# Optimization experiments

Hardware: AMD Instinct MI355X
Metric: run time of the kernel (lower is better)

The kernel has to match this reference:

```python
import jax, jax.numpy as jnp
import numpy as np

NUM_HEADS = 16
MASKED_BIAS = -10000.0


def setup_inputs() -> dict:
    key = jax.random.key(0)
    k1, k2, k3 = jax.random.split(key, 3)
    B, S, D = 4, 2048, 1024
    scale = 0.02
    return {
        "hidden_states": jax.random.normal(k1, (B, S, D), dtype=jnp.float32),
        "c_attn_w": jax.random.normal(k2, (D, 3 * D), dtype=jnp.float32) * scale,
        "c_attn_b": jnp.zeros((3 * D,), dtype=jnp.float32),
        "c_proj_w": jax.random.normal(k3, (D, D), dtype=jnp.float32) * scale,
        "c_proj_b": jnp.zeros((D,), dtype=jnp.float32),
    }


def reference(hidden_states, c_attn_w, c_attn_b, c_proj_w, c_proj_b):
    B, S, D = hidden_states.shape
    H = NUM_HEADS
    hd = D // H
    # qkv projection (HF Conv1D: x @ W + b)
    qkv = hidden_states @ c_attn_w + c_attn_b  # [B, S, 3D]
    q, k, v = jnp.split(qkv, 3, axis=-1)

    def split_heads(t):
        return t.reshape(B, S, H, hd).transpose(0, 2, 1, 3)  # [B, H, S, hd]

    q, k, v = split_heads(q), split_heads(k), split_heads(v)
    # full score matrix [B, H, S, S] (eager attention)
    attn = jnp.einsum("bhqd,bhkd->bhqk", q, k) / jnp.sqrt(jnp.float32(hd))
    causal = jnp.tril(jnp.ones((S, S), dtype=bool))  # [S, S]
    attn = jnp.where(causal[None, None], attn, jnp.float32(MASKED_BIAS))
    attn = jax.nn.softmax(attn, axis=-1)
    out = jnp.einsum("bhqk,bhkd->bhqd", attn, v)  # [B, H, S, hd]
    out = out.transpose(0, 2, 1, 3).reshape(B, S, D)  # merge heads
    out = out @ c_proj_w + c_proj_b
    return out
```

## Files before the change

kernel.cpp:

```cpp
#include <hip/hip_runtime.h>

#define NH 16
#define HD 64

typedef __attribute__((ext_vector_type(8))) _Float16 f16x8;
typedef __attribute__((ext_vector_type(4))) float f32x4;
typedef __attribute__((ext_vector_type(8))) unsigned short us8;
typedef __attribute__((ext_vector_type(4))) unsigned short us4;
typedef __attribute__((ext_vector_type(2))) unsigned int u32x2;

#define CEXP 0.18033688f

__device__ __forceinline__ unsigned short f2h(float f) {
    _Float16 h = (_Float16)f;
    return __builtin_bit_cast(unsigned short, h);
}

__global__ __launch_bounds__(256)
void cast_f16(const float* __restrict__ in, unsigned short* __restrict__ out) {
    size_t i = ((size_t)blockIdx.x * 256 + threadIdx.x) * 4;
    float4 v = *reinterpret_cast<const float4*>(in + i);
    us4 w;
    w[0] = f2h(v.x); w[1] = f2h(v.y); w[2] = f2h(v.z); w[3] = f2h(v.w);
    *reinterpret_cast<us4*>(out + i) = w;
}

__global__ __launch_bounds__(256)
void transpose_cast(const float* __restrict__ in, unsigned short* __restrict__ out,
                    int R, int C) {
    __shared__ float T[64][65];
    const int c0 = blockIdx.x * 64, r0 = blockIdx.y * 64;
    const int tid = threadIdx.x;
    const int rr = tid >> 4, cc4 = (tid & 15) * 4;
    #pragma unroll
    for (int p = 0; p < 4; ++p) {
        int r = rr + p * 16;
        float4 v = *reinterpret_cast<const float4*>(
            in + (size_t)(r0 + r) * C + c0 + cc4);
        T[r][cc4] = v.x; T[r][cc4 + 1] = v.y; T[r][cc4 + 2] = v.z; T[r][cc4 + 3] = v.w;
    }
    __syncthreads();
    #pragma unroll
    for (int p = 0; p < 4; ++p) {
        int orow = rr + p * 16;
        us4 w;
        #pragma unroll
        for (int j = 0; j < 4; ++j) w[j] = f2h(T[cc4 + j][orow]);
        *reinterpret_cast<us4*>(out + (size_t)(c0 + orow) * R + r0 + cc4) = w;
    }
}

__device__ __forceinline__ void stage128(unsigned short* dst,
                                         const unsigned short* src, int stride) {
    const int tid = threadIdx.x;
    #pragma unroll
    for (int p = 0; p < 4; ++p) {
        int idx = tid + p * 256;
        int r = idx >> 3;
        int slot = idx & 7;
        us8 v = *reinterpret_cast<const us8*>(src + (size_t)r * stride + slot * 8);
        int cb = (slot << 4) ^ ((r & 7) << 4);
        *reinterpret_cast<us8*>(reinterpret_cast<char*>(dst) + r * 128 + cb) = v;
    }
}

__device__ __forceinline__ void stage64(unsigned short* dst,
                                        const unsigned short* src, int stride) {
    const int tid = threadIdx.x;
    #pragma unroll
    for (int p = 0; p < 2; ++p) {
        int idx = tid + p * 256;
        int r = idx >> 3;
        int slot = idx & 7;
        us8 v = *reinterpret_cast<const us8*>(src + (size_t)r * stride + slot * 8);
        int cb = (slot << 4) ^ ((r & 7) << 4);
        *reinterpret_cast<us8*>(reinterpret_cast<char*>(dst) + r * 128 + cb) = v;
    }
}

__device__ __forceinline__ f16x8 frag16(const unsigned short* base, int row0, int ks) {
    const int lane = threadIdx.x & 63;
    const int r = row0 + (lane & 15);
    int cb = ((ks << 6) + (lane & 48)) ^ ((r & 7) << 4);
    return *reinterpret_cast<const f16x8*>(
        reinterpret_cast<const char*>(base) + r * 128 + cb);
}

template<int MODE>
__global__ __launch_bounds__(256)
void gemm_f16(const unsigned short* __restrict__ A,
              const unsigned short* __restrict__ Bt,
              const float* __restrict__ bias,
              float* __restrict__ C,
              unsigned short* __restrict__ qb,
              unsigned short* __restrict__ kb,
              unsigned short* __restrict__ vtb,
              int M, int N, int K) {
    __shared__ __align__(16) unsigned short As[128 * 64];
    __shared__ __align__(16) unsigned short Bs[128 * 64];

    const int tid = threadIdx.x;
    const int wid = tid >> 6, lane = tid & 63, g = lane >> 4;
    const int wr = wid >> 1, wc = wid & 1;
    const int m0 = blockIdx.y * 128, n0 = blockIdx.x * 128;

    f32x4 acc[4][4];
    #pragma unroll
    for (int i = 0; i < 4; ++i)
        #pragma unroll
        for (int j = 0; j < 4; ++j) {
            acc[i][j][0] = 0.f; acc[i][j][1] = 0.f;
            acc[i][j][2] = 0.f; acc[i][j][3] = 0.f;
        }

    for (int k0 = 0; k0 < K; k0 += 64) {
        __syncthreads();
        stage128(As, A + (size_t)m0 * K + k0, K);
        stage128(Bs, Bt + (size_t)n0 * K + k0, K);
        __syncthreads();

        f16x8 af[4][2], bf[4][2];
        #pragma unroll
        for (int mi = 0; mi < 4; ++mi)
            #pragma unroll
            for (int ks = 0; ks < 2; ++ks)
                af[mi][ks] = frag16(As, wr * 64 + mi * 16, ks);
        #pragma unroll
        for (int ni = 0; ni < 4; ++ni)
            #pragma unroll
            for (int ks = 0; ks < 2; ++ks)
                bf[ni][ks] = frag16(Bs, wc * 64 + ni * 16, ks);

        __builtin_amdgcn_s_setprio(1);
        #pragma unroll
        for (int ks = 0; ks < 2; ++ks)
            #pragma unroll
            for (int mi = 0; mi < 4; ++mi)
                #pragma unroll
                for (int ni = 0; ni < 4; ++ni)
                    acc[mi][ni] = __builtin_amdgcn_mfma_f32_16x16x32_f16(
                        af[mi][ks], bf[ni][ks], acc[mi][ni], 0, 0, 0);
        __builtin_amdgcn_s_setprio(0);
    }

    const int colBase = n0 + wc * 64;
    const int rowBase = m0 + wr * 64;

    if (MODE == 0) {
        #pragma unroll
        for (int ni = 0; ni < 4; ++ni) {
            int col = colBase + ni * 16 + (lane & 15);
            float bv = bias[col];
            #pragma unroll
            for (int mi = 0; mi < 4; ++mi) {
                int row = rowBase + mi * 16 + g * 4;
                #pragma unroll
                for (int reg = 0; reg < 4; ++reg)
                    C[(size_t)(row + reg) * N + col] = acc[mi][ni][reg] + bv;
            }
        }
    } else {
        #pragma unroll
        for (int ni = 0; ni < 4; ++ni) {
            int col = colBase + ni * 16 + (lane & 15);
            float bv = bias[col];
            int seg = col >> 10;
            int cc = col & 1023;
            int h = cc >> 6, d = cc & 63;
            const float sc = (seg == 0) ? CEXP : 1.0f;
            #pragma unroll
            for (int mi = 0; mi < 4; ++mi) {
                int row = rowBase + mi * 16 + g * 4;
                int b = row >> 11, s = row & 2047;
                size_t bh = (size_t)(b * NH + h);
                if (seg < 2) {
                    unsigned short* dst = (seg ? kb : qb)
                        + bh * 2048 * 64 + (size_t)s * 64 + d;
                    #pragma unroll
                    for (int reg = 0; reg < 4; ++reg)
                        dst[(size_t)reg * 64] = f2h((acc[mi][ni][reg] + bv) * sc);
                } else {
                    unsigned short* dst = vtb
                        + bh * 64 * 2048 + (size_t)d * 2048 + s;
                    us4 w;
                    #pragma unroll
                    for (int reg = 0; reg < 4; ++reg)
                        w[reg] = f2h(acc[mi][ni][reg] + bv);
                    *reinterpret_cast<us4*>(dst) = w;
                }
            }
        }
    }
}

template<bool DIAG>
__device__ __forceinline__ void attn_tile(
    f16x8 qf0, f16x8 qf1,
    const unsigned short* Ks, const unsigned short* Vs, unsigned short* Pw,
    f32x4 (&o)[4], float& l_,
    int kt, int qrow_base, int lane, int g) {

    f32x4 s[4];
    #pragma unroll
    for (int n = 0; n < 4; ++n) { s[n][0] = 0.f; s[n][1] = 0.f; s[n][2] = 0.f; s[n][3] = 0.f; }

    __builtin_amdgcn_s_setprio(1);
    #pragma unroll
    for (int ks = 0; ks < 2; ++ks) {
        f16x8 b = ks ? qf1 : qf0;
        #pragma unroll
        for (int n = 0; n < 4; ++n)
            s[n] = __builtin_amdgcn_mfma_f32_16x16x32_f16(
                frag16(Ks, n * 16, ks), b, s[n], 0, 0, 0);
    }
    __builtin_amdgcn_s_setprio(0);

    const int q = lane & 15;
    float psum = 0.f;
    #pragma unroll
    for (int n = 0; n < 4; ++n) {
        float p0 = __builtin_exp2f(s[n][0]);
        float p1 = __builtin_exp2f(s[n][1]);
        float p2 = __builtin_exp2f(s[n][2]);
        float p3 = __builtin_exp2f(s[n][3]);
        if (DIAG) {
            const int kb_ = kt * 64 + (g << 2) + 16 * n;
            const int qg = qrow_base + q;
            p0 = (kb_ + 0 > qg) ? 0.f : p0;
            p1 = (kb_ + 1 > qg) ? 0.f : p1;
            p2 = (kb_ + 2 > qg) ? 0.f : p2;
            p3 = (kb_ + 3 > qg) ? 0.f : p3;
        }
        psum += (p0 + p1) + (p2 + p3);
        u32x2 w;
        w[0] = __builtin_bit_cast(unsigned int, __builtin_amdgcn_cvt_pkrtz(p0, p1));
        w[1] = __builtin_bit_cast(unsigned int, __builtin_amdgcn_cvt_pkrtz(p2, p3));
        int pcb = ((n << 5) + (g << 3)) ^ ((q & 7) << 4);
        *reinterpret_cast<u32x2*>(
            reinterpret_cast<char*>(Pw) + q * 128 + pcb) = w;
    }
    l_ += psum;

    __builtin_amdgcn_s_setprio(1);
    #pragma unroll
    for (int ks = 0; ks < 2; ++ks) {
        f16x8 pa = frag16(Pw, 0, ks);
        #pragma unroll
        for (int n = 0; n < 4; ++n)
            o[n] = __builtin_amdgcn_mfma_f32_16x16x32_f16(
                pa, frag16(Vs, n * 16, ks), o[n], 0, 0, 0);
    }
    __builtin_amdgcn_s_setprio(0);
}

__global__ __launch_bounds__(256, 4)
void attn_mfma(const unsigned short* __restrict__ qb,
               const unsigned short* __restrict__ kb,
               const unsigned short* __restrict__ vtb,
               unsigned short* __restrict__ attno) {
    const int f = blockIdx.x;
    const int xcd = f & 7;
    const int wi = f >> 3;
    const int bh = xcd * 8 + (wi >> 4);
    const int pair = wi & 15;
    const int qtA = pair, qtB = 31 - pair;
    const int tid = threadIdx.x;
    const int wid = tid >> 6, lane = tid & 63, g = lane >> 4;

    __shared__ __align__(16) unsigned short Ks[64 * 64];
    __shared__ __align__(16) unsigned short Vs[64 * 64];
    __shared__ __align__(16) unsigned short Ps[4][16 * 64];

    const unsigned short* kg0 = kb + (size_t)bh * 2048 * 64;
    const unsigned short* vg0 = vtb + (size_t)bh * 64 * 2048;

    const int qrl = wid * 16 + (lane & 15);
    const int qd0 = (lane >> 4) * 8;
    const unsigned short* qbase = qb + (size_t)bh * 2048 * 64;
    f16x8 qA0 = *reinterpret_cast<const f16x8*>(qbase + (size_t)(qtA * 64 + qrl) * 64 + qd0);
    f16x8 qA1 = *reinterpret_cast<const f16x8*>(qbase + (size_t)(qtA * 64 + qrl) * 64 + 32 + qd0);
    f16x8 qB0 = *reinterpret_cast<const f16x8*>(qbase + (size_t)(qtB * 64 + qrl) * 64 + qd0);
    f16x8 qB1 = *reinterpret_cast<const f16x8*>(qbase + (size_t)(qtB * 64 + qrl) * 64 + 32 + qd0);

    f32x4 oA[4], oB[4];
    float lA = 0.f, lB = 0.f;
    #pragma unroll
    for (int n = 0; n < 4; ++n) {
        #pragma unroll
        for (int r = 0; r < 4; ++r) { oA[n][r] = 0.f; oB[n][r] = 0.f; }
    }

    unsigned short* Pw = Ps[wid];
    const int qrbA = qtA * 64 + wid * 16;
    const int qrbB = qtB * 64 + wid * 16;

    auto STAGE = [&](int kt) {
        __syncthreads();
        stage64(Ks, kg0 + (size_t)kt * 64 * 64, 64);
        stage64(Vs, vg0 + (size_t)kt * 64, 2048);
        __syncthreads();
    };

    for (int kt = 0; kt < qtA; ++kt) {
        STAGE(kt);
        attn_tile<false>(qB0, qB1, Ks, Vs, Pw, oB, lB, kt, qrbB, lane, g);
        attn_tile<false>(qA0, qA1, Ks, Vs, Pw, oA, lA, kt, qrbA, lane, g);
    }
    STAGE(qtA);
    attn_tile<false>(qB0, qB1, Ks, Vs, Pw, oB, lB, qtA, qrbB, lane, g);
    attn_tile<true >(qA0, qA1, Ks, Vs, Pw, oA, lA, qtA, qrbA, lane, g);
    for (int kt = qtA + 1; kt < qtB; ++kt) {
        STAGE(kt);
        attn_tile<false>(qB0, qB1, Ks, Vs, Pw, oB, lB, kt, qrbB, lane, g);
    }
    STAGE(qtB);
    attn_tile<true >(qB0, qB1, Ks, Vs, Pw, oB, lB, qtB, qrbB, lane, g);

    const int b = bh >> 4, h = bh & 15;
    #pragma unroll
    for (int ph = 0; ph < 2; ++ph) {
        const int qt = ph ? qtB : qtA;
        f32x4* o = ph ? oB : oA;
        float ltot = ph ? lB : lA;
        ltot += __shfl_xor(ltot, 16);
        ltot += __shfl_xor(ltot, 32);
        unsigned short* ob = attno
            + (size_t)(b * 2048 + qt * 64 + wid * 16) * 1024 + h * 64;
        #pragma unroll
        for (int reg = 0; reg < 4; ++reg) {
            int row = (g << 2) + reg;
            float inv = 1.0f / __shfl(ltot, row);
            #pragma unroll
            for (int n = 0; n < 4; ++n)
                ob[(size_t)row * 1024 + n * 16 + (lane & 15)] = f2h(o[n][reg] * inv);
        }
    }
}

extern "C" void kernel_launch(void* const* d_in, const int* in_sizes, int n_in,
                              void* d_out, int out_size, void* d_ws, size_t ws_size,
                              hipStream_t stream) {
    const float* x    = (const float*)d_in[0];
    const float* Wqkv = (const float*)d_in[1];
    const float* bqkv = (const float*)d_in[2];
    const float* Wp   = (const float*)d_in[3];
    const float* bp   = (const float*)d_in[4];
    float* out = (float*)d_out;

    const int B = 4, S = 2048, D = 1024;
    const int M = B * S;
    const size_t HSZ = (size_t)M * D;

    unsigned short* xh    = (unsigned short*)d_ws;
    unsigned short* wqt   = xh + HSZ;
    unsigned short* wpt   = wqt + (size_t)3 * D * D;
    unsigned short* qbuf  = wpt + (size_t)D * D;
    unsigned short* kbuf  = qbuf + HSZ;
    unsigned short* vtb   = kbuf + HSZ;
    unsigned short* attno = vtb + HSZ;

    dim3 blk(256);
    cast_f16<<<dim3((int)(HSZ / 1024)), blk, 0, stream>>>(x, xh);
    transpose_cast<<<dim3(3 * D / 64, D / 64), blk, 0, stream>>>(Wqkv, wqt, D, 3 * D);
    transpose_cast<<<dim3(D / 64, D / 64), blk, 0, stream>>>(Wp, wpt, D, D);

    gemm_f16<1><<<dim3(3 * D / 128, M / 128), blk, 0, stream>>>(
        xh, wqt, bqkv, nullptr, qbuf, kbuf, vtb, M, 3 * D, D);
    attn_mfma<<<dim3(1024), blk, 0, stream>>>(qbuf, kbuf, vtb, attno);
    gemm_f16<0><<<dim3(D / 128, M / 128), blk, 0, stream>>>(
        attno, wpt, bp, out, nullptr, nullptr, nullptr, M, D, D);
}
```

Before: 182.9 us.

## Fuse input cast into QKV GEMM and double-buffer attention K/V via async LDS loads

Removes the standalone fp32->fp16 cast kernel by converting x on the fly while staging A tiles in the QKV GEMM. The attention kernel now double-buffers K and V tiles using global_load_lds direct-to-LDS loads with source-side swizzling, prefetching the next tile while computing the current one and cutting barriers per tile. Trade-offs: the GEMM reads fp32 activations (twice the bytes per A tile, repeated across column blocks), and uses round-toward-zero conversion.

Result: slower. 228.3 us (+24.8%).

```diff
diff --git a/kernel.cpp b/kernel.cpp
--- a/kernel.cpp
+++ b/kernel.cpp
@@ -16,14 +16,9 @@
     return __builtin_bit_cast(unsigned short, h);
 }
 
-__global__ __launch_bounds__(256)
-void cast_f16(const float* __restrict__ in, unsigned short* __restrict__ out) {
-    size_t i = ((size_t)blockIdx.x * 256 + threadIdx.x) * 4;
-    float4 v = *reinterpret_cast<const float4*>(in + i);
-    us4 w;
-    w[0] = f2h(v.x); w[1] = f2h(v.y); w[2] = f2h(v.z); w[3] = f2h(v.w);
-    *reinterpret_cast<us4*>(out + i) = w;
-}
+#define GL16(gp, lp) __builtin_amdgcn_global_load_lds(                        \
+    (const __attribute__((address_space(1))) void*)(gp),                      \
+    (__attribute__((address_space(3))) void*)(lp), 16, 0, 0)
 
 __global__ __launch_bounds__(256)
 void transpose_cast(const float* __restrict__ in, unsigned short* __restrict__ out,
@@ -64,17 +59,24 @@
     }
 }
 
-__device__ __forceinline__ void stage64(unsigned short* dst,
-                                        const unsigned short* src, int stride) {
-    const int tid = threadIdx.x;
-    #pragma unroll
-    for (int p = 0; p < 2; ++p) {
+__device__ __forceinline__ void stage128_f32(unsigned short* dst,
+                                             const float* src, int stride) {
+    const int tid = threadIdx.x;
+    #pragma unroll
+    for (int p = 0; p < 4; ++p) {
         int idx = tid + p * 256;
         int r = idx >> 3;
         int slot = idx & 7;
-        us8 v = *reinterpret_cast<const us8*>(src + (size_t)r * stride + slot * 8);
+        const float* s = src + (size_t)r * stride + slot * 8;
+        float4 a = *reinterpret_cast<const float4*>(s);
+        float4 b = *reinterpret_cast<const float4*>(s + 4);
+        uint4 w;
+        w.x = __builtin_bit_cast(unsigned int, __builtin_amdgcn_cvt_pkrtz(a.x, a.y));
+        w.y = __builtin_bit_cast(unsigned int, __builtin_amdgcn_cvt_pkrtz(a.z, a.w));
+        w.z = __builtin_bit_cast(unsigned int, __builtin_amdgcn_cvt_pkrtz(b.x, b.y));
+        w.w = __builtin_bit_cast(unsigned int, __builtin_amdgcn_cvt_pkrtz(b.z, b.w));
         int cb = (slot << 4) ^ ((r & 7) << 4);
-        *reinterpret_cast<us8*>(reinterpret_cast<char*>(dst) + r * 128 + cb) = v;
+        *reinterpret_cast<uint4*>(reinterpret_cast<char*>(dst) + r * 128 + cb) = w;
     }
 }
 
@@ -88,7 +90,7 @@
 
 template<int MODE>
 __global__ __launch_bounds__(256)
-void gemm_f16(const unsigned short* __restrict__ A,
+void gemm_f16(const void* __restrict__ Ax,
               const unsigned short* __restrict__ Bt,
               const float* __restrict__ bias,
               float* __restrict__ C,
@@ -115,7 +117,10 @@
 
     for (int k0 = 0; k0 < K; k0 += 64) {
         __syncthreads();
-        stage128(As, A + (size_t)m0 * K + k0, K);
+        if (MODE == 1)
+            stage128_f32(As, (const float*)Ax + (size_t)m0 * K + k0, K);
+        else
+            stage128(As, (const unsigned short*)Ax + (size_t)m0 * K + k0, K);
         stage128(Bs, Bt + (size_t)n0 * K + k0, K);
         __syncthreads();
 
@@ -267,12 +272,12 @@
     const int tid = threadIdx.x;
     const int wid = tid >> 6, lane = tid & 63, g = lane >> 4;
 
-    __shared__ __align__(16) unsigned short Ks[64 * 64];
-    __shared__ __align__(16) unsigned short Vs[64 * 64];
+    __shared__ __align__(16) unsigned short Ks[2][64 * 64];
+    __shared__ __align__(16) unsigned short Vs[2][64 * 64];
     __shared__ __align__(16) unsigned short Ps[4][16 * 64];
 
-    const unsigned short* kg0 = kb + (size_t)bh * 2048 * 64;
-    const unsigned short* vg0 = vtb + (size_t)bh * 64 * 2048;
+    const char* kg0 = (const char*)(kb + (size_t)bh * 2048 * 64);
+    const char* vg0 = (const char*)(vtb + (size_t)bh * 64 * 2048);
 
     const int qrl = wid * 16 + (lane & 15);
     const int qd0 = (lane >> 4) * 8;
@@ -294,27 +299,42 @@
     const int qrbA = qtA * 64 + wid * 16;
     const int qrbB = qtB * 64 + wid * 16;
 
-    auto STAGE = [&](int kt) {
+    auto PREF = [&](int kt, int buf) {
+        const char* kb_ = kg0 + (size_t)kt * 8192;
+        const char* vb_ = vg0 + (size_t)kt * 128;
+        #pragma unroll
+        for (int i = 0; i < 2; ++i) {
+            int rbase = wid * 16 + i * 8;
+            int row = rbase + (lane >> 3);
+            int gs = (lane & 7) ^ (row & 7);
+            GL16(kb_ + (size_t)row * 128 + gs * 16,
+                 (char*)Ks[buf] + rbase * 128);
+            GL16(vb_ + (size_t)row * 4096 + gs * 16,
+                 (char*)Vs[buf] + rbase * 128);
+        }
+    };
+
+    PREF(0, 0);
+    __syncthreads();
+    int cur = 0;
+    for (int kt = 0; kt <= qtB; ++kt) {
+        if (kt < qtB) PREF(kt + 1, cur ^ 1);
+        const unsigned short* Kc = Ks[cur];
+        const unsigned short* Vc = Vs[cur];
+        if (kt < qtA) {
+            attn_tile<false>(qB0, qB1, Kc, Vc, Pw, oB, lB, kt, qrbB, lane, g);
+            attn_tile<false>(qA0, qA1, Kc, Vc, Pw, oA, lA, kt, qrbA, lane, g);
+        } else if (kt == qtA) {
+            attn_tile<false>(qB0, qB1, Kc, Vc, Pw, oB, lB, kt, qrbB, lane, g);
+            attn_tile<true >(qA0, qA1, Kc, Vc, Pw, oA, lA, kt, qrbA, lane, g);
+        } else if (kt < qtB) {
+            attn_tile<false>(qB0, qB1, Kc, Vc, Pw, oB, lB, kt, qrbB, lane, g);
+        } else {
+            attn_tile<true >(qB0, qB1, Kc, Vc, Pw, oB, lB, kt, qrbB, lane, g);
+        }
         __syncthreads();
-        stage64(Ks, kg0 + (size_t)kt * 64 * 64, 64);
-        stage64(Vs, vg0 + (size_t)kt * 64, 2048);
-        __syncthreads();
-    };
-
-    for (int kt = 0; kt < qtA; ++kt) {
-        STAGE(kt);
-        attn_tile<false>(qB0, qB1, Ks, Vs, Pw, oB, lB, kt, qrbB, lane, g);
-        attn_tile<false>(qA0, qA1, Ks, Vs, Pw, oA, lA, kt, qrbA, lane, g);
-    }
-    STAGE(qtA);
-    attn_tile<false>(qB0, qB1, Ks, Vs, Pw, oB, lB, qtA, qrbB, lane, g);
-    attn_tile<true >(qA0, qA1, Ks, Vs, Pw, oA, lA, qtA, qrbA, lane, g);
-    for (int kt = qtA + 1; kt < qtB; ++kt) {
-        STAGE(kt);
-        attn_tile<false>(qB0, qB1, Ks, Vs, Pw, oB, lB, kt, qrbB, lane, g);
-    }
-    STAGE(qtB);
-    attn_tile<true >(qB0, qB1, Ks, Vs, Pw, oB, lB, qtB, qrbB, lane, g);
+        cur ^= 1;
+    }
 
     const int b = bh >> 4, h = bh & 15;
     #pragma unroll
@@ -351,8 +371,7 @@
     const int M = B * S;
     const size_t HSZ = (size_t)M * D;
 
-    unsigned short* xh    = (unsigned short*)d_ws;
-    unsigned short* wqt   = xh + HSZ;
+    unsigned short* wqt   = (unsigned short*)d_ws;
     unsigned short* wpt   = wqt + (size_t)3 * D * D;
     unsigned short* qbuf  = wpt + (size_t)D * D;
     unsigned short* kbuf  = qbuf + HSZ;
@@ -360,12 +379,11 @@
     unsigned short* attno = vtb + HSZ;
 
     dim3 blk(256);
-    cast_f16<<<dim3((int)(HSZ / 1024)), blk, 0, stream>>>(x, xh);
     transpose_cast<<<dim3(3 * D / 64, D / 64), blk, 0, stream>>>(Wqkv, wqt, D, 3 * D);
     transpose_cast<<<dim3(D / 64, D / 64), blk, 0, stream>>>(Wp, wpt, D, D);
 
     gemm_f16<1><<<dim3(3 * D / 128, M / 128), blk, 0, stream>>>(
-        xh, wqt, bqkv, nullptr, qbuf, kbuf, vtb, M, 3 * D, D);
+        x, wqt, bqkv, nullptr, qbuf, kbuf, vtb, M, 3 * D, D);
     attn_mfma<<<dim3(1024), blk, 0, stream>>>(qbuf, kbuf, vtb, attno);
     gemm_f16<0><<<dim3(D / 128, M / 128), blk, 0, stream>>>(
         attno, wpt, bp, out, nullptr, nullptr, nullptr, M, D, D);
```
